# Kernel optimization log

Hardware: AMD Instinct MI355X
Metric: run time of the kernel (lower is better)

The kernel has to match this reference:

```python
import jax, jax.numpy as jnp
import numpy as np

B, T, D, H = 8, 4096, 256, 256

def setup_inputs() -> dict:
    key = jax.random.key(0)
    ks = jax.random.split(key, 6)
    scale = 1.0 / np.sqrt(D)
    return {
        "x": jax.random.normal(ks[0], (B, T, D), dtype=jnp.float32),
        "h0": jax.random.normal(ks[1], (B, H), dtype=jnp.float32),
        "Wz": jax.random.normal(ks[2], (H, D), dtype=jnp.float32) * scale,
        "bz": jax.random.normal(ks[3], (H,), dtype=jnp.float32) * scale,
        "Wh": jax.random.normal(ks[4], (H, D), dtype=jnp.float32) * scale,
        "bh": jax.random.normal(ks[5], (H,), dtype=jnp.float32) * scale,
    }

def reference(x, h0, Wz, bz, Wh, bh):
    # gate and update depend only on the input (minGRU): compute in one shot
    gate = jax.nn.sigmoid(jnp.einsum("btd,hd->bth", x, Wz) + bz)   # [B,T,H]
    update = jnp.einsum("btd,hd->bth", x, Wh) + bh                  # [B,T,H]

    def step(h, gu):
        g, u = gu
        h_new = (1.0 - g) * h + g * u
        return h_new, h_new

    # scan over time; xs laid out [T,B,H]
    _, hs = jax.lax.scan(step, h0, (jnp.swapaxes(gate, 0, 1), jnp.swapaxes(update, 0, 1)))
    return jnp.swapaxes(hs, 0, 1)  # [B,T,H]
```

## Files before the change

### kernel.cpp

```cpp
#include <hip/hip_runtime.h>
#include <hip/hip_fp16.h>


namespace {
constexpr int kB  = 8;
constexpr int kT  = 4096;
constexpr int kD  = 256;
constexpr int kH  = 256;
constexpr int kBT = kB * kT;
constexpr int kL  = 32;
constexpr int kNC = kT / kL;

constexpr int TM  = 128;
constexpr int TH  = 64;
constexpr int BK  = 64;
}

typedef short s16x8 __attribute__((ext_vector_type(8)));
typedef short s16x4 __attribute__((ext_vector_type(4)));
typedef float f32x4 __attribute__((ext_vector_type(4)));

__device__ __forceinline__ short f2bf(float f) {
    union { float f; unsigned int u; } v; v.f = f;
    unsigned int r = v.u + 0x7fffu + ((v.u >> 16) & 1u);
    return (short)(r >> 16);
}

__device__ __forceinline__ void load_lds16(const void* g, void* l) {
    __builtin_amdgcn_global_load_lds(
        (const __attribute__((address_space(1))) void*)g,
        (__attribute__((address_space(3))) void*)l, 16, 0, 0);
}

__global__ __launch_bounds__(256)
void convert_bf16(const float* __restrict__ x,
                  const float* __restrict__ Wz,
                  const float* __restrict__ Wh,
                  unsigned short* __restrict__ xb,
                  unsigned short* __restrict__ wzb,
                  unsigned short* __restrict__ whb)
{
    constexpr int X4 = kBT * kD / 4;
    constexpr int W4 = kH  * kD / 4;
    const int i = blockIdx.x * 256 + threadIdx.x;
    const float* src; unsigned short* dst; int j;
    if (i < X4)           { src = x;  dst = xb;  j = i; }
    else if (i < X4 + W4) { src = Wz; dst = wzb; j = i - X4; }
    else                  { src = Wh; dst = whb; j = i - X4 - W4; }
    const float4 v = ((const float4*)src)[j];
    s16x4 p;
    p[0] = f2bf(v.x); p[1] = f2bf(v.y); p[2] = f2bf(v.z); p[3] = f2bf(v.w);
    ((s16x4*)dst)[j] = p;
}

__global__ __launch_bounds__(256)
void gemm_fused(const unsigned short* __restrict__ xb,
                const unsigned short* __restrict__ wzb,
                const unsigned short* __restrict__ whb,
                const float* __restrict__ bz,
                const float* __restrict__ bh,
                __half2* __restrict__ ab_ws,
                float2* __restrict__ ABsum)
{
    __shared__ __align__(16) unsigned char smem[32768];
    unsigned short* Xs  = (unsigned short*)smem;
    unsigned short* Wzs = Xs  + 128 * 64;
    unsigned short* Whs = Wzs + 64 * 64;
    __half* a_lds = (__half*)smem;
    __half* b_lds = a_lds + 128 * 64;

    const int tid  = threadIdx.x;
    const int lane = tid & 63;
    const int wv   = tid >> 6;
    const int ln15 = lane & 15;
    const int quad = lane >> 4;
    const int wr0  = (wv & 1) * 64;
    const int wc0  = (wv >> 1) * 32;
    const int row0 = blockIdx.y * TM;
    const int col0 = blockIdx.x * TH;

    const int srow = lane >> 3;
    const int sk   = (lane & 7) * 8;

    f32x4 accZ[4][2] = {};
    f32x4 accU[4][2] = {};

    for (int k0 = 0; k0 < kD; k0 += BK) {
        #pragma unroll
        for (int s = 0; s < 4; ++s) {
            const int seg = wv * 4 + s;
            const int m = seg * 8 + srow;
            load_lds16(xb + (size_t)(row0 + m) * kD + k0 + sk, Xs + seg * 512);
        }
        #pragma unroll
        for (int s = 0; s < 2; ++s) {
            const int seg = wv * 2 + s;
            const int m = seg * 8 + srow;
            load_lds16(wzb + (size_t)(col0 + m) * kD + k0 + sk, Wzs + seg * 512);
            load_lds16(whb + (size_t)(col0 + m) * kD + k0 + sk, Whs + seg * 512);
        }
        __syncthreads();

        #pragma unroll
        for (int kk = 0; kk < BK; kk += 32) {
            s16x8 af[4], bzf[2], buf[2];
            #pragma unroll
            for (int mt = 0; mt < 4; ++mt)
                af[mt] = *(const s16x8*)&Xs[(wr0 + mt * 16 + ln15) * 64 + kk + quad * 8];
            #pragma unroll
            for (int nt = 0; nt < 2; ++nt) {
                bzf[nt] = *(const s16x8*)&Wzs[(wc0 + nt * 16 + ln15) * 64 + kk + quad * 8];
                buf[nt] = *(const s16x8*)&Whs[(wc0 + nt * 16 + ln15) * 64 + kk + quad * 8];
            }
            #pragma unroll
            for (int mt = 0; mt < 4; ++mt) {
                #pragma unroll
                for (int nt = 0; nt < 2; ++nt) {
                    accZ[mt][nt] = __builtin_amdgcn_mfma_f32_16x16x32_bf16(
                        af[mt], bzf[nt], accZ[mt][nt], 0, 0, 0);
                    accU[mt][nt] = __builtin_amdgcn_mfma_f32_16x16x32_bf16(
                        af[mt], buf[nt], accU[mt][nt], 0, 0, 0);
                }
            }
        }
        __syncthreads();
    }

    #pragma unroll
    for (int nt = 0; nt < 2; ++nt) {
        const int col = col0 + wc0 + nt * 16 + ln15;
        const int lc  = wc0 + nt * 16 + ln15;
        const float bzv = bz[col];
        const float bhv = bh[col];
        #pragma unroll
        for (int mt = 0; mt < 4; ++mt) {
            const int rb = wr0 + mt * 16 + quad * 4;
            #pragma unroll
            for (int r = 0; r < 4; ++r) {
                const float z = accZ[mt][nt][r] + bzv;
                const float g = 1.0f / (1.0f + __expf(-z));
                const float u = accU[mt][nt][r] + bhv;
                a_lds[(rb + r) * 64 + lc] = __float2half_rn(1.0f - g);
                b_lds[(rb + r) * 64 + lc] = __float2half_rn(g * u);
            }
        }
    }
    __syncthreads();

    #pragma unroll
    for (int it = 0; it < 16; ++it) {
        const int q  = tid + it * 256;
        const int t  = q >> 5;
        const int hp = (q & 31) * 2;
        const __half a0 = a_lds[t * 64 + hp],     a1 = a_lds[t * 64 + hp + 1];
        const __half b0 = b_lds[t * 64 + hp],     b1 = b_lds[t * 64 + hp + 1];
        __half2 v0, v1;
        v0 = __halves2half2(a0, b0);
        v1 = __halves2half2(a1, b1);
        __half2* dst = ab_ws + (size_t)(row0 + t) * kH + col0 + hp;
        dst[0] = v0; dst[1] = v1;
    }

    {
        const int s = tid >> 6;
        const int h = tid & 63;
        float A = 1.0f, Bv = 0.0f;
        #pragma unroll 8
        for (int t = s * 32; t < s * 32 + 32; ++t) {
            const float a  = __half2float(a_lds[t * 64 + h]);
            const float bb = __half2float(b_lds[t * 64 + h]);
            Bv = fmaf(a, Bv, bb);
            A *= a;
        }
        const int b = row0 / kT;
        const int c = (row0 % kT) / kL + s;
        float2 o; o.x = A; o.y = Bv;
        ABsum[(size_t)(b * kNC + c) * kH + col0 + h] = o;
    }
}

__global__ __launch_bounds__(256)
void combine(const float* __restrict__ h0,
             const float2* __restrict__ ABsum,
             float* __restrict__ hstart)
{
    const int b = blockIdx.x;
    const int h = threadIdx.x;
    float hv = h0[(size_t)b * kH + h];
    #pragma unroll 8
    for (int c = 0; c < kNC; ++c) {
        const size_t idx = (size_t)(b * kNC + c) * kH + h;
        hstart[idx] = hv;
        const float2 ab = ABsum[idx];
        hv = fmaf(ab.x, hv, ab.y);
    }
}

__global__ __launch_bounds__(256)
void apply_scan(const __half2* __restrict__ ab_ws,
                const float* __restrict__ hstart,
                float* __restrict__ out)
{
    const int c = blockIdx.x & (kNC - 1);
    const int b = blockIdx.x >> 7;
    const int h = threadIdx.x;

    float hv = hstart[(size_t)(b * kNC + c) * kH + h];
    const size_t base = ((size_t)b * kT + (size_t)c * kL) * kH + h;
    #pragma unroll 8
    for (int t = 0; t < kL; ++t) {
        const __half2 ab = ab_ws[base + (size_t)t * kH];
        hv = fmaf(__low2float(ab), hv, __high2float(ab));
        out[base + (size_t)t * kH] = hv;
    }
}

extern "C" void kernel_launch(void* const* d_in, const int* in_sizes, int n_in,
                              void* d_out, int out_size, void* d_ws, size_t ws_size,
                              hipStream_t stream)
{
    const float* x  = (const float*)d_in[0];
    const float* h0 = (const float*)d_in[1];
    const float* Wz = (const float*)d_in[2];
    const float* bz = (const float*)d_in[3];
    const float* Wh = (const float*)d_in[4];
    const float* bh = (const float*)d_in[5];
    float* out = (float*)d_out;

    unsigned char* ws = (unsigned char*)d_ws;
    unsigned short* xb  = (unsigned short*)ws;                 ws += (size_t)kBT * kD * 2;
    unsigned short* wzb = (unsigned short*)ws;                 ws += (size_t)kH * kD * 2;
    unsigned short* whb = (unsigned short*)ws;                 ws += (size_t)kH * kD * 2;
    __half2* ab_ws      = (__half2*)ws;                        ws += (size_t)kBT * kH * 4;
    float2* ABsum       = (float2*)ws;                         ws += (size_t)kB * kNC * kH * 8;
    float* hstart       = (float*)ws;

    constexpr int CV_BLOCKS = (kBT * kD / 4 + 2 * (kH * kD / 4)) / 256;
    convert_bf16<<<CV_BLOCKS, 256, 0, stream>>>(x, Wz, Wh, xb, wzb, whb);
    gemm_fused<<<dim3(kH / TH, kBT / TM), 256, 0, stream>>>(
        xb, wzb, whb, bz, bh, ab_ws, ABsum);
    combine<<<kB, kH, 0, stream>>>(h0, ABsum, hstart);
    apply_scan<<<kB * kNC, kH, 0, stream>>>(ab_ws, hstart, out);
}
```

Before: 132.0 us.

## Fuse bf16 conversion into GEMM loads with padded LDS tiles

Removes the separate convert_bf16 kernel and its bf16 workspace. The GEMM now reads fp32 x and weights directly into registers, converts them to bf16, and stores them into LDS tiles padded to reduce bank conflicts. The epilogue LDS stride is also padded, and launch bounds request 3 blocks per CU. The cost is that each of the 4 column blocks re-reads fp32 x (twice the bytes of bf16), and the register-staged loads replace the direct global-to-LDS copies with an extra sync per k step.

```diff
diff --git a/kernel.cpp b/kernel.cpp
--- a/kernel.cpp
+++ b/kernel.cpp
@@ -14,6 +14,8 @@
 constexpr int TM  = 128;
 constexpr int TH  = 64;
 constexpr int BK  = 64;
+constexpr int LDP = 72;
+constexpr int EPS = 66;
 }
 
 typedef short s16x8 __attribute__((ext_vector_type(8)));
@@ -25,49 +27,27 @@
     unsigned int r = v.u + 0x7fffu + ((v.u >> 16) & 1u);
     return (short)(r >> 16);
 }
-
-__device__ __forceinline__ void load_lds16(const void* g, void* l) {
-    __builtin_amdgcn_global_load_lds(
-        (const __attribute__((address_space(1))) void*)g,
-        (__attribute__((address_space(3))) void*)l, 16, 0, 0);
-}
-
-__global__ __launch_bounds__(256)
-void convert_bf16(const float* __restrict__ x,
-                  const float* __restrict__ Wz,
-                  const float* __restrict__ Wh,
-                  unsigned short* __restrict__ xb,
-                  unsigned short* __restrict__ wzb,
-                  unsigned short* __restrict__ whb)
-{
-    constexpr int X4 = kBT * kD / 4;
-    constexpr int W4 = kH  * kD / 4;
-    const int i = blockIdx.x * 256 + threadIdx.x;
-    const float* src; unsigned short* dst; int j;
-    if (i < X4)           { src = x;  dst = xb;  j = i; }
-    else if (i < X4 + W4) { src = Wz; dst = wzb; j = i - X4; }
-    else                  { src = Wh; dst = whb; j = i - X4 - W4; }
-    const float4 v = ((const float4*)src)[j];
+__device__ __forceinline__ s16x4 cvt4(float4 v) {
     s16x4 p;
     p[0] = f2bf(v.x); p[1] = f2bf(v.y); p[2] = f2bf(v.z); p[3] = f2bf(v.w);
-    ((s16x4*)dst)[j] = p;
-}
-
-__global__ __launch_bounds__(256)
-void gemm_fused(const unsigned short* __restrict__ xb,
-                const unsigned short* __restrict__ wzb,
-                const unsigned short* __restrict__ whb,
+    return p;
+}
+
+__global__ __launch_bounds__(256, 3)
+void gemm_fused(const float* __restrict__ x,
+                const float* __restrict__ Wz,
                 const float* __restrict__ bz,
+                const float* __restrict__ Wh,
                 const float* __restrict__ bh,
                 __half2* __restrict__ ab_ws,
                 float2* __restrict__ ABsum)
 {
-    __shared__ __align__(16) unsigned char smem[32768];
+    __shared__ __align__(16) unsigned char smem[36864];
     unsigned short* Xs  = (unsigned short*)smem;
-    unsigned short* Wzs = Xs  + 128 * 64;
-    unsigned short* Whs = Wzs + 64 * 64;
+    unsigned short* Wzs = Xs  + 128 * LDP;
+    unsigned short* Whs = Wzs + 64 * LDP;
     __half* a_lds = (__half*)smem;
-    __half* b_lds = a_lds + 128 * 64;
+    __half* b_lds = a_lds + 128 * EPS;
 
     const int tid  = threadIdx.x;
     const int lane = tid & 63;
@@ -79,25 +59,31 @@
     const int row0 = blockIdx.y * TM;
     const int col0 = blockIdx.x * TH;
 
-    const int srow = lane >> 3;
-    const int sk   = (lane & 7) * 8;
+    const int srow = tid >> 4;
+    const int sc4  = (tid & 15) * 4;
 
     f32x4 accZ[4][2] = {};
     f32x4 accU[4][2] = {};
 
     for (int k0 = 0; k0 < kD; k0 += BK) {
-        #pragma unroll
-        for (int s = 0; s < 4; ++s) {
-            const int seg = wv * 4 + s;
-            const int m = seg * 8 + srow;
-            load_lds16(xb + (size_t)(row0 + m) * kD + k0 + sk, Xs + seg * 512);
-        }
-        #pragma unroll
-        for (int s = 0; s < 2; ++s) {
-            const int seg = wv * 2 + s;
-            const int m = seg * 8 + srow;
-            load_lds16(wzb + (size_t)(col0 + m) * kD + k0 + sk, Wzs + seg * 512);
-            load_lds16(whb + (size_t)(col0 + m) * kD + k0 + sk, Whs + seg * 512);
+        float4 xv[8], wzv[4], whv[4];
+        #pragma unroll
+        for (int p = 0; p < 8; ++p)
+            xv[p] = *(const float4*)(x + (size_t)(row0 + p * 16 + srow) * kD + k0 + sc4);
+        #pragma unroll
+        for (int p = 0; p < 4; ++p) {
+            wzv[p] = *(const float4*)(Wz + (size_t)(col0 + p * 16 + srow) * kD + k0 + sc4);
+            whv[p] = *(const float4*)(Wh + (size_t)(col0 + p * 16 + srow) * kD + k0 + sc4);
+        }
+        __syncthreads();
+
+        #pragma unroll
+        for (int p = 0; p < 8; ++p)
+            *(s16x4*)&Xs[(p * 16 + srow) * LDP + sc4] = cvt4(xv[p]);
+        #pragma unroll
+        for (int p = 0; p < 4; ++p) {
+            *(s16x4*)&Wzs[(p * 16 + srow) * LDP + sc4] = cvt4(wzv[p]);
+            *(s16x4*)&Whs[(p * 16 + srow) * LDP + sc4] = cvt4(whv[p]);
         }
         __syncthreads();
 
@@ -106,11 +92,11 @@
             s16x8 af[4], bzf[2], buf[2];
             #pragma unroll
             for (int mt = 0; mt < 4; ++mt)
-                af[mt] = *(const s16x8*)&Xs[(wr0 + mt * 16 + ln15) * 64 + kk + quad * 8];
+                af[mt] = *(const s16x8*)&Xs[(wr0 + mt * 16 + ln15) * LDP + kk + quad * 8];
             #pragma unroll
             for (int nt = 0; nt < 2; ++nt) {
-                bzf[nt] = *(const s16x8*)&Wzs[(wc0 + nt * 16 + ln15) * 64 + kk + quad * 8];
-                buf[nt] = *(const s16x8*)&Whs[(wc0 + nt * 16 + ln15) * 64 + kk + quad * 8];
+                bzf[nt] = *(const s16x8*)&Wzs[(wc0 + nt * 16 + ln15) * LDP + kk + quad * 8];
+                buf[nt] = *(const s16x8*)&Whs[(wc0 + nt * 16 + ln15) * LDP + kk + quad * 8];
             }
             #pragma unroll
             for (int mt = 0; mt < 4; ++mt) {
@@ -123,8 +109,8 @@
                 }
             }
         }
-        __syncthreads();
-    }
+    }
+    __syncthreads();
 
     #pragma unroll
     for (int nt = 0; nt < 2; ++nt) {
@@ -140,8 +126,8 @@
                 const float z = accZ[mt][nt][r] + bzv;
                 const float g = 1.0f / (1.0f + __expf(-z));
                 const float u = accU[mt][nt][r] + bhv;
-                a_lds[(rb + r) * 64 + lc] = __float2half_rn(1.0f - g);
-                b_lds[(rb + r) * 64 + lc] = __float2half_rn(g * u);
+                a_lds[(rb + r) * EPS + lc] = __float2half_rn(1.0f - g);
+                b_lds[(rb + r) * EPS + lc] = __float2half_rn(g * u);
             }
         }
     }
@@ -152,13 +138,11 @@
         const int q  = tid + it * 256;
         const int t  = q >> 5;
         const int hp = (q & 31) * 2;
-        const __half a0 = a_lds[t * 64 + hp],     a1 = a_lds[t * 64 + hp + 1];
-        const __half b0 = b_lds[t * 64 + hp],     b1 = b_lds[t * 64 + hp + 1];
-        __half2 v0, v1;
-        v0 = __halves2half2(a0, b0);
-        v1 = __halves2half2(a1, b1);
+        const __half a0 = a_lds[t * EPS + hp],     a1 = a_lds[t * EPS + hp + 1];
+        const __half b0 = b_lds[t * EPS + hp],     b1 = b_lds[t * EPS + hp + 1];
         __half2* dst = ab_ws + (size_t)(row0 + t) * kH + col0 + hp;
-        dst[0] = v0; dst[1] = v1;
+        dst[0] = __halves2half2(a0, b0);
+        dst[1] = __halves2half2(a1, b1);
     }
 
     {
@@ -167,8 +151,8 @@
         float A = 1.0f, Bv = 0.0f;
         #pragma unroll 8
         for (int t = s * 32; t < s * 32 + 32; ++t) {
-            const float a  = __half2float(a_lds[t * 64 + h]);
-            const float bb = __half2float(b_lds[t * 64 + h]);
+            const float a  = __half2float(a_lds[t * EPS + h]);
+            const float bb = __half2float(b_lds[t * EPS + h]);
             Bv = fmaf(a, Bv, bb);
             A *= a;
         }
@@ -228,17 +212,12 @@
     float* out = (float*)d_out;
 
     unsigned char* ws = (unsigned char*)d_ws;
-    unsigned short* xb  = (unsigned short*)ws;                 ws += (size_t)kBT * kD * 2;
-    unsigned short* wzb = (unsigned short*)ws;                 ws += (size_t)kH * kD * 2;
-    unsigned short* whb = (unsigned short*)ws;                 ws += (size_t)kH * kD * 2;
-    __half2* ab_ws      = (__half2*)ws;                        ws += (size_t)kBT * kH * 4;
-    float2* ABsum       = (float2*)ws;                         ws += (size_t)kB * kNC * kH * 8;
-    float* hstart       = (float*)ws;
-
-    constexpr int CV_BLOCKS = (kBT * kD / 4 + 2 * (kH * kD / 4)) / 256;
-    convert_bf16<<<CV_BLOCKS, 256, 0, stream>>>(x, Wz, Wh, xb, wzb, whb);
+    __half2* ab_ws = (__half2*)ws;        ws += (size_t)kBT * kH * 4;
+    float2* ABsum  = (float2*)ws;         ws += (size_t)kB * kNC * kH * 8;
+    float* hstart  = (float*)ws;
+
     gemm_fused<<<dim3(kH / TH, kBT / TM), 256, 0, stream>>>(
-        xb, wzb, whb, bz, bh, ab_ws, ABsum);
+        x, Wz, bz, Wh, bh, ab_ws, ABsum);
     combine<<<kB, kH, 0, stream>>>(h0, ABsum, hstart);
     apply_scan<<<kB * kNC, kH, 0, stream>>>(ab_ws, hstart, out);
 }
```

Result: slower. 155.8 us (+18.0%).

## Fuse GEMM and chunked scan via decoupled lookback across time tiles

Applied to the files above, without the earlier changes.

The separate combine and apply_scan kernels are removed. Each GEMM block now computes its tile's gate and update values, publishes a per-tile scan aggregate through flagged 64-bit atomics, and spins on its predecessors' aggregates to obtain the starting hidden state. It then writes the final outputs directly, so the fp16 intermediate buffer never goes to global memory. The LDS row stride is padded to 66 to cut bank conflicts, and the aggregate flags are zeroed inside the prologue kernel. The lookback depends on blocks being scheduled in order along time, and each block's serial walk over earlier tiles grows with its position in the sequence.

```diff
diff --git a/kernel.cpp b/kernel.cpp
--- a/kernel.cpp
+++ b/kernel.cpp
@@ -8,12 +8,13 @@
 constexpr int kD  = 256;
 constexpr int kH  = 256;
 constexpr int kBT = kB * kT;
-constexpr int kL  = 32;
-constexpr int kNC = kT / kL;
 
 constexpr int TM  = 128;
 constexpr int TH  = 64;
 constexpr int BK  = 64;
+constexpr int kNT = kT / TM;
+constexpr int kNChain = kB * (kH / TH);
+constexpr int EPS = 66;
 }
 
 typedef short s16x8 __attribute__((ext_vector_type(8)));
@@ -33,16 +34,24 @@
 }
 
 __global__ __launch_bounds__(256)
-void convert_bf16(const float* __restrict__ x,
-                  const float* __restrict__ Wz,
-                  const float* __restrict__ Wh,
-                  unsigned short* __restrict__ xb,
-                  unsigned short* __restrict__ wzb,
-                  unsigned short* __restrict__ whb)
+void prologue(const float* __restrict__ x,
+              const float* __restrict__ Wz,
+              const float* __restrict__ Wh,
+              unsigned short* __restrict__ xb,
+              unsigned short* __restrict__ wzb,
+              unsigned short* __restrict__ whb,
+              float4* __restrict__ aggz)
 {
     constexpr int X4 = kBT * kD / 4;
     constexpr int W4 = kH  * kD / 4;
+    constexpr int Z4 = kNChain * kNT * TH * 8 / 16;
     const int i = blockIdx.x * 256 + threadIdx.x;
+
+    if (i >= X4 + 2 * W4) {
+        float4 z; z.x = 0.f; z.y = 0.f; z.z = 0.f; z.w = 0.f;
+        aggz[i - (X4 + 2 * W4)] = z;
+        return;
+    }
     const float* src; unsigned short* dst; int j;
     if (i < X4)           { src = x;  dst = xb;  j = i; }
     else if (i < X4 + W4) { src = Wz; dst = wzb; j = i - X4; }
@@ -53,21 +62,24 @@
     ((s16x4*)dst)[j] = p;
 }
 
-__global__ __launch_bounds__(256)
-void gemm_fused(const unsigned short* __restrict__ xb,
-                const unsigned short* __restrict__ wzb,
-                const unsigned short* __restrict__ whb,
-                const float* __restrict__ bz,
-                const float* __restrict__ bh,
-                __half2* __restrict__ ab_ws,
-                float2* __restrict__ ABsum)
+__global__ __launch_bounds__(256, 4)
+void gemm_scan_fused(const unsigned short* __restrict__ xb,
+                     const unsigned short* __restrict__ wzb,
+                     const unsigned short* __restrict__ whb,
+                     const float* __restrict__ bz,
+                     const float* __restrict__ bh,
+                     const float* __restrict__ h0,
+                     unsigned long long* __restrict__ agg,
+                     float* __restrict__ out)
 {
-    __shared__ __align__(16) unsigned char smem[32768];
+    __shared__ __align__(16) unsigned char smem[36096];
     unsigned short* Xs  = (unsigned short*)smem;
     unsigned short* Wzs = Xs  + 128 * 64;
     unsigned short* Whs = Wzs + 64 * 64;
-    __half* a_lds = (__half*)smem;
-    __half* b_lds = a_lds + 128 * 64;
+    __half* a_lds   = (__half*)smem;
+    __half* b_lds   = a_lds + 128 * EPS;
+    float2* sub_lds = (float2*)(smem + 33792);
+    float*  hs_lds  = (float*)(smem + 35840);
 
     const int tid  = threadIdx.x;
     const int lane = tid & 63;
@@ -76,8 +88,12 @@
     const int quad = lane >> 4;
     const int wr0  = (wv & 1) * 64;
     const int wc0  = (wv >> 1) * 32;
-    const int row0 = blockIdx.y * TM;
-    const int col0 = blockIdx.x * TH;
+
+    const int chain = blockIdx.x;
+    const int t     = blockIdx.y;
+    const int b     = chain >> 2;
+    const int col0  = (chain & 3) * TH;
+    const int row0  = b * kT + t * TM;
 
     const int srow = lane >> 3;
     const int sk   = (lane & 7) * 8;
@@ -140,78 +156,72 @@
                 const float z = accZ[mt][nt][r] + bzv;
                 const float g = 1.0f / (1.0f + __expf(-z));
                 const float u = accU[mt][nt][r] + bhv;
-                a_lds[(rb + r) * 64 + lc] = __float2half_rn(1.0f - g);
-                b_lds[(rb + r) * 64 + lc] = __float2half_rn(g * u);
+                a_lds[(rb + r) * EPS + lc] = __float2half_rn(1.0f - g);
+                b_lds[(rb + r) * EPS + lc] = __float2half_rn(g * u);
             }
         }
     }
     __syncthreads();
 
-    #pragma unroll
-    for (int it = 0; it < 16; ++it) {
-        const int q  = tid + it * 256;
-        const int t  = q >> 5;
-        const int hp = (q & 31) * 2;
-        const __half a0 = a_lds[t * 64 + hp],     a1 = a_lds[t * 64 + hp + 1];
-        const __half b0 = b_lds[t * 64 + hp],     b1 = b_lds[t * 64 + hp + 1];
-        __half2 v0, v1;
-        v0 = __halves2half2(a0, b0);
-        v1 = __halves2half2(a1, b1);
-        __half2* dst = ab_ws + (size_t)(row0 + t) * kH + col0 + hp;
-        dst[0] = v0; dst[1] = v1;
-    }
-
+    const int s = tid >> 6;
+    const int h = tid & 63;
     {
-        const int s = tid >> 6;
-        const int h = tid & 63;
         float A = 1.0f, Bv = 0.0f;
         #pragma unroll 8
-        for (int t = s * 32; t < s * 32 + 32; ++t) {
-            const float a  = __half2float(a_lds[t * 64 + h]);
-            const float bb = __half2float(b_lds[t * 64 + h]);
+        for (int r = s * 32; r < s * 32 + 32; ++r) {
+            const float a  = __half2float(a_lds[r * EPS + h]);
+            const float bb = __half2float(b_lds[r * EPS + h]);
             Bv = fmaf(a, Bv, bb);
             A *= a;
         }
-        const int b = row0 / kT;
-        const int c = (row0 % kT) / kL + s;
         float2 o; o.x = A; o.y = Bv;
-        ABsum[(size_t)(b * kNC + c) * kH + col0 + h] = o;
-    }
-}
-
-__global__ __launch_bounds__(256)
-void combine(const float* __restrict__ h0,
-             const float2* __restrict__ ABsum,
-             float* __restrict__ hstart)
-{
-    const int b = blockIdx.x;
-    const int h = threadIdx.x;
-    float hv = h0[(size_t)b * kH + h];
-    #pragma unroll 8
-    for (int c = 0; c < kNC; ++c) {
-        const size_t idx = (size_t)(b * kNC + c) * kH + h;
-        hstart[idx] = hv;
-        const float2 ab = ABsum[idx];
-        hv = fmaf(ab.x, hv, ab.y);
-    }
-}
-
-__global__ __launch_bounds__(256)
-void apply_scan(const __half2* __restrict__ ab_ws,
-                const float* __restrict__ hstart,
-                float* __restrict__ out)
-{
-    const int c = blockIdx.x & (kNC - 1);
-    const int b = blockIdx.x >> 7;
-    const int h = threadIdx.x;
-
-    float hv = hstart[(size_t)(b * kNC + c) * kH + h];
-    const size_t base = ((size_t)b * kT + (size_t)c * kL) * kH + h;
-    #pragma unroll 8
-    for (int t = 0; t < kL; ++t) {
-        const __half2 ab = ab_ws[base + (size_t)t * kH];
-        hv = fmaf(__low2float(ab), hv, __high2float(ab));
-        out[base + (size_t)t * kH] = hv;
+        sub_lds[s * 64 + h] = o;
+    }
+    __syncthreads();
+
+    if (tid < 64) {
+        float A = 1.0f, Bv = 0.0f;
+        #pragma unroll
+        for (int s2 = 0; s2 < 4; ++s2) {
+            const float2 g = sub_lds[s2 * 64 + tid];
+            Bv = fmaf(g.x, Bv, g.y);
+            A *= g.x;
+        }
+        union { float2 f; unsigned long long u; } pk;
+        pk.f.x = A; pk.f.y = Bv;
+        pk.u |= 1ull;
+        __hip_atomic_store(&agg[(size_t)(chain * kNT + t) * 64 + tid], pk.u,
+                           __ATOMIC_RELAXED, __HIP_MEMORY_SCOPE_AGENT);
+
+        float hs = h0[(size_t)b * kH + col0 + tid];
+        for (int j = 0; j < t; ++j) {
+            unsigned long long u;
+            do {
+                u = __hip_atomic_load(&agg[(size_t)(chain * kNT + j) * 64 + tid],
+                                      __ATOMIC_RELAXED, __HIP_MEMORY_SCOPE_AGENT);
+            } while (u == 0ull);
+            union { unsigned long long u; float2 f; } qk; qk.u = u;
+            hs = fmaf(qk.f.x, hs, qk.f.y);
+        }
+        hs_lds[tid] = hs;
+    }
+    __syncthreads();
+
+    {
+        float hv = hs_lds[h];
+        #pragma unroll
+        for (int s2 = 0; s2 < s; ++s2) {
+            const float2 g = sub_lds[s2 * 64 + h];
+            hv = fmaf(g.x, hv, g.y);
+        }
+        #pragma unroll 8
+        for (int r = 0; r < 32; ++r) {
+            const int lr = s * 32 + r;
+            const float a  = __half2float(a_lds[lr * EPS + h]);
+            const float bb = __half2float(b_lds[lr * EPS + h]);
+            hv = fmaf(a, hv, bb);
+            out[(size_t)(row0 + lr) * kH + col0 + h] = hv;
+        }
     }
 }
 
@@ -228,17 +238,15 @@
     float* out = (float*)d_out;
 
     unsigned char* ws = (unsigned char*)d_ws;
-    unsigned short* xb  = (unsigned short*)ws;                 ws += (size_t)kBT * kD * 2;
-    unsigned short* wzb = (unsigned short*)ws;                 ws += (size_t)kH * kD * 2;
-    unsigned short* whb = (unsigned short*)ws;                 ws += (size_t)kH * kD * 2;
-    __half2* ab_ws      = (__half2*)ws;                        ws += (size_t)kBT * kH * 4;
-    float2* ABsum       = (float2*)ws;                         ws += (size_t)kB * kNC * kH * 8;
-    float* hstart       = (float*)ws;
-
-    constexpr int CV_BLOCKS = (kBT * kD / 4 + 2 * (kH * kD / 4)) / 256;
-    convert_bf16<<<CV_BLOCKS, 256, 0, stream>>>(x, Wz, Wh, xb, wzb, whb);
-    gemm_fused<<<dim3(kH / TH, kBT / TM), 256, 0, stream>>>(
-        xb, wzb, whb, bz, bh, ab_ws, ABsum);
-    combine<<<kB, kH, 0, stream>>>(h0, ABsum, hstart);
-    apply_scan<<<kB * kNC, kH, 0, stream>>>(ab_ws, hstart, out);
-}
+    unsigned short* xb  = (unsigned short*)ws;   ws += (size_t)kBT * kD * 2;
+    unsigned short* wzb = (unsigned short*)ws;   ws += (size_t)kH * kD * 2;
+    unsigned short* whb = (unsigned short*)ws;   ws += (size_t)kH * kD * 2;
+    unsigned long long* agg = (unsigned long long*)ws;
+
+    constexpr int PRO_ITEMS = kBT * kD / 4 + 2 * (kH * kD / 4)
+                            + kNChain * kNT * TH * 8 / 16;
+    prologue<<<PRO_ITEMS / 256, 256, 0, stream>>>(
+        x, Wz, Wh, xb, wzb, whb, (float4*)agg);
+    gemm_scan_fused<<<dim3(kNChain, kNT), 256, 0, stream>>>(
+        xb, wzb, whb, bz, bh, h0, agg, out);
+}
```

Result: faster. 118.1 us (-10.6%).
